# Kernel optimization log

Hardware: AMD Instinct MI355X
Metric: run time of the kernel (lower is better)

The kernel has to match this reference:

```python
import jax, jax.numpy as jnp
import numpy as np

B, C, H, W = 8, 3, 1024, 1024
N_SPOTS = int(H * W * 0.015)  # 15728, matches torch: n = int(H*W*0.015)
KSIZE, SIGMA = 5, 1.5
RMAX = 3  # max snow-box radius (torch.randint(1, 4))


def setup_inputs() -> dict:
    key = jax.random.key(0)
    k1, k2, k3, k4 = jax.random.split(key, 4)
    x = jax.random.uniform(k1, (B, C, H, W), dtype=jnp.float32)
    ys = jax.random.randint(k2, (B, N_SPOTS), 0, H)
    xs = jax.random.randint(k3, (B, N_SPOTS), 0, W)
    rs = jax.random.randint(k4, (B, N_SPOTS), 0, 3)  # radius = rs + 1 in {1,2,3}
    return {"x": x, "ys": ys, "xs": xs, "rs": rs}


def _snow_mask(ys, xs, rs, h, w):
    # Union of axis-aligned boxes: pixel (py,px) is snow iff some spot has
    # |py - y| <= r and |px - x| <= r (box clipping to the image is equivalent).
    b, n = ys.shape
    r = rs + 1  # radii 1..3
    d = jnp.arange(-RMAX, RMAX + 1)
    dy = jnp.repeat(d, 2 * RMAX + 1)  # [49]
    dx = jnp.tile(d, 2 * RMAX + 1)    # [49]
    yy = ys[:, :, None] + dy  # [B, n, 49]
    xx = xs[:, :, None] + dx
    valid = ((jnp.abs(dy) <= r[:, :, None]) & (jnp.abs(dx) <= r[:, :, None])
             & (yy >= 0) & (yy < h) & (xx >= 0) & (xx < w))
    yy = jnp.where(valid, yy, h)  # out-of-bounds sentinel -> dropped by scatter
    xx = jnp.where(valid, xx, w)
    b_idx = jnp.broadcast_to(jnp.arange(b)[:, None, None], yy.shape)
    mask = jnp.zeros((b, h, w), dtype=bool)
    mask = mask.at[b_idx, yy, xx].set(True, mode="drop")
    return mask


def _gauss_kernel():
    coords = jnp.arange(KSIZE, dtype=jnp.float32) - KSIZE // 2
    g = jnp.exp(-coords ** 2 / (2.0 * SIGMA ** 2))
    g = g / g.sum()
    return jnp.outer(g, g)  # [5, 5]


def reference(x, ys, xs, rs):
    b, c, h, w = x.shape
    mask = _snow_mask(ys, xs, rs, h, w)                   # [B, H, W]
    out = jnp.where(mask[:, None, :, :], jnp.float32(0.95), x)
    kernel = jnp.broadcast_to(_gauss_kernel(), (c, 1, KSIZE, KSIZE))  # depthwise OIHW
    pad = KSIZE // 2
    out = jax.lax.conv_general_dilated(
        out, kernel, window_strides=(1, 1), padding=[(pad, pad), (pad, pad)],
        dimension_numbers=("NCHW", "OIHW", "NCHW"), feature_group_count=c)
    return jnp.clip(out, 0.0, 1.0)
```

## Files before the change

kernel.cpp:

```cpp
#include <hip/hip_runtime.h>

#define BB 8
#define CC 3
#define HH 1024
#define WW 1024
#define NS 15728

#define G0 0.1200784f
#define G1 0.2338808f
#define G2 0.2920816f

__global__ __launch_bounds__(256) void snow_mask_kernel(
    const int* __restrict__ ys, const int* __restrict__ xs,
    const int* __restrict__ rs, unsigned int* __restrict__ mbits) {
  int s = blockIdx.x * 256 + threadIdx.x;
  if (s >= NS) return;
  int b = blockIdx.y;
  int idx = b * NS + s;
  int y = ys[idx];
  int x = xs[idx];
  int r = rs[idx] + 1;
  int x0 = max(x - r, 0), x1 = min(x + r, WW - 1);
  int y0 = max(y - r, 0), y1 = min(y + r, HH - 1);
  int w0 = x0 >> 5, w1 = x1 >> 5;
  unsigned int m0 = 0xFFFFFFFFu << (x0 & 31);
  unsigned int m1 = 0xFFFFFFFFu >> (31 - (x1 & 31));
  for (int py = y0; py <= y1; ++py) {
    unsigned int* rowp = mbits + ((unsigned)(b * HH + py) << 5);
    if (w0 == w1) {
      atomicOr(&rowp[w0], m0 & m1);
    } else {
      atomicOr(&rowp[w0], m0);
      atomicOr(&rowp[w1], m1);
    }
  }
}

__device__ __forceinline__ float hpass5(const float* row, int tx) {
  return G0 * (row[tx + 2] + row[tx + 6]) +
         G1 * (row[tx + 3] + row[tx + 5]) +
         G2 * row[tx + 4];
}

__global__ __launch_bounds__(256) void snow_blur_kernel(
    const float* __restrict__ x, const unsigned int* __restrict__ mbits,
    float* __restrict__ out) {
  __shared__ float tile[68][72];

  const int bz = blockIdx.z;
  const int b = bz / CC;
  const int bx = blockIdx.x, by = blockIdx.y;
  const int tid = threadIdx.x;
  const float* __restrict__ xp = x + (size_t)bz * (HH * WW);
  const unsigned int* __restrict__ mb = mbits + ((unsigned)(b * HH) << 5);

  const int gxbase = bx * 64 - 4;
  const int gybase = by * 64 - 2;

  const bool interior = (bx > 0) & (bx < 15) & (by > 0) & (by < 15);
  if (interior) {
#pragma unroll
    for (int k = 0; k < 5; ++k) {
      int i = tid + k * 256;
      if (i < 1224) {
        int r = i / 18;
        int c4 = i - r * 18;
        int gy = gybase + r;
        int gx = gxbase + c4 * 4;
        float4 v = *(const float4*)(xp + (size_t)gy * WW + gx);
        unsigned int mword = mb[(gy << 5) + (gx >> 5)];
        unsigned int bits = (mword >> (gx & 31)) & 0xFu;
        if (bits & 1u) v.x = 0.95f;
        if (bits & 2u) v.y = 0.95f;
        if (bits & 4u) v.z = 0.95f;
        if (bits & 8u) v.w = 0.95f;
        *(float4*)&tile[r][c4 * 4] = v;
      }
    }
  } else {
    for (int i = tid; i < 68 * 72; i += 256) {
      int r = i / 72;
      int c = i - r * 72;
      int gy = gybase + r;
      int gx = gxbase + c;
      float v = 0.f;
      if (gy >= 0 && gy < HH && gx >= 0 && gx < WW) {
        v = xp[(size_t)gy * WW + gx];
        if ((mb[(gy << 5) + (gx >> 5)] >> (gx & 31)) & 1u) v = 0.95f;
      }
      tile[r][c] = v;
    }
  }
  __syncthreads();

  const int tx = tid & 63;
  const int ty = tid >> 6;
  const int rbase = ty * 16;

  float h0 = hpass5(tile[rbase + 0], tx);
  float h1 = hpass5(tile[rbase + 1], tx);
  float h2 = hpass5(tile[rbase + 2], tx);
  float h3 = hpass5(tile[rbase + 3], tx);
  float h4 = hpass5(tile[rbase + 4], tx);

  size_t obase = (size_t)bz * (HH * WW) +
                 (size_t)(by * 64 + rbase) * WW +
                 (size_t)(bx * 64 + tx);
#pragma unroll
  for (int k = 0; k < 16; ++k) {
    float s = G0 * (h0 + h4) + G1 * (h1 + h3) + G2 * h2;
    s = fminf(fmaxf(s, 0.f), 1.f);
    out[obase + (size_t)k * WW] = s;
    h0 = h1; h1 = h2; h2 = h3; h3 = h4;
    if (k < 15) h4 = hpass5(tile[rbase + k + 5], tx);
  }
}

extern "C" void kernel_launch(void* const* d_in, const int* in_sizes, int n_in,
                              void* d_out, int out_size, void* d_ws, size_t ws_size,
                              hipStream_t stream) {
  const float* x = (const float*)d_in[0];
  const int* ys = (const int*)d_in[1];
  const int* xs = (const int*)d_in[2];
  const int* rs = (const int*)d_in[3];
  float* out = (float*)d_out;

  unsigned int* mbits = (unsigned int*)d_ws;
  hipMemsetAsync(mbits, 0, (size_t)BB * HH * WW / 8, stream);

  dim3 mgrid((NS + 255) / 256, BB);
  snow_mask_kernel<<<mgrid, 256, 0, stream>>>(ys, xs, rs, mbits);

  dim3 grid(WW / 64, HH / 64, BB * CC);
  snow_blur_kernel<<<grid, 256, 0, stream>>>(x, mbits, out);
}
```

Before: 230.9 us.

## Widen blur tiles to 128 columns with float4 per-thread outputs and clamped loads

The blur kernel now covers a 128x64 tile per block. Each thread computes four adjacent output columns over eight rows, using vectorized LDS reads and float4 global stores. The separate boundary path is replaced by clamped loads with a zero-out flag, and all ten loads are issued before the shared-memory writes so more memory requests are in flight. This cuts halo overhead and instruction count per output, but raises register pressure, which the added occupancy hint of 4 may constrain.

```diff
diff --git a/kernel.cpp b/kernel.cpp
--- a/kernel.cpp
+++ b/kernel.cpp
@@ -36,16 +36,13 @@
   }
 }
 
-__device__ __forceinline__ float hpass5(const float* row, int tx) {
-  return G0 * (row[tx + 2] + row[tx + 6]) +
-         G1 * (row[tx + 3] + row[tx + 5]) +
-         G2 * row[tx + 4];
-}
+#define TS 140
+#define NLOAD 2312
 
-__global__ __launch_bounds__(256) void snow_blur_kernel(
+__global__ __launch_bounds__(256, 4) void snow_blur_kernel(
     const float* __restrict__ x, const unsigned int* __restrict__ mbits,
     float* __restrict__ out) {
-  __shared__ float tile[68][72];
+  __shared__ float tile[68 * TS];
 
   const int bz = blockIdx.z;
   const int b = bz / CC;
@@ -54,65 +51,76 @@
   const float* __restrict__ xp = x + (size_t)bz * (HH * WW);
   const unsigned int* __restrict__ mb = mbits + ((unsigned)(b * HH) << 5);
 
-  const int gxbase = bx * 64 - 4;
+  const int gxbase = bx * 128 - 4;
   const int gybase = by * 64 - 2;
 
-  const bool interior = (bx > 0) & (bx < 15) & (by > 0) & (by < 15);
-  if (interior) {
+  float4 v[10];
+  unsigned int bits[10];
+  int lidx[10];
 #pragma unroll
-    for (int k = 0; k < 5; ++k) {
-      int i = tid + k * 256;
-      if (i < 1224) {
-        int r = i / 18;
-        int c4 = i - r * 18;
-        int gy = gybase + r;
-        int gx = gxbase + c4 * 4;
-        float4 v = *(const float4*)(xp + (size_t)gy * WW + gx);
-        unsigned int mword = mb[(gy << 5) + (gx >> 5)];
-        unsigned int bits = (mword >> (gx & 31)) & 0xFu;
-        if (bits & 1u) v.x = 0.95f;
-        if (bits & 2u) v.y = 0.95f;
-        if (bits & 4u) v.z = 0.95f;
-        if (bits & 8u) v.w = 0.95f;
-        *(float4*)&tile[r][c4 * 4] = v;
-      }
-    }
-  } else {
-    for (int i = tid; i < 68 * 72; i += 256) {
-      int r = i / 72;
-      int c = i - r * 72;
-      int gy = gybase + r;
-      int gx = gxbase + c;
-      float v = 0.f;
-      if (gy >= 0 && gy < HH && gx >= 0 && gx < WW) {
-        v = xp[(size_t)gy * WW + gx];
-        if ((mb[(gy << 5) + (gx >> 5)] >> (gx & 31)) & 1u) v = 0.95f;
-      }
-      tile[r][c] = v;
-    }
+  for (int k = 0; k < 10; ++k) {
+    int i = tid + k * 256;
+    i = i < (NLOAD - 1) ? i : (NLOAD - 1);
+    int r = i / 34;
+    int c4 = i - r * 34;
+    int gy = gybase + r;
+    int gx = gxbase + c4 * 4;
+    int gyc = min(max(gy, 0), HH - 1);
+    int gxc = min(max(gx, 0), WW - 4);
+    v[k] = *(const float4*)(xp + (size_t)gyc * WW + gxc);
+    unsigned int bm = (mb[(gyc << 5) + (gxc >> 5)] >> (gxc & 31)) & 0xFu;
+    if ((gy != gyc) | (gx != gxc)) bm = 16u;
+    bits[k] = bm;
+    lidx[k] = r * TS + c4 * 4;
+  }
+#pragma unroll
+  for (int k = 0; k < 10; ++k) {
+    float4 t = v[k];
+    unsigned int bm = bits[k];
+    if (bm & 1u) t.x = 0.95f;
+    if (bm & 2u) t.y = 0.95f;
+    if (bm & 4u) t.z = 0.95f;
+    if (bm & 8u) t.w = 0.95f;
+    if (bm & 16u) { t.x = 0.f; t.y = 0.f; t.z = 0.f; t.w = 0.f; }
+    *(float4*)&tile[lidx[k]] = t;
   }
   __syncthreads();
 
-  const int tx = tid & 63;
-  const int ty = tid >> 6;
-  const int rbase = ty * 16;
+  const int c = tid & 31;
+  const int ty = tid >> 5;
+  const float* trow = tile + (ty * 8) * TS + c * 4;
 
-  float h0 = hpass5(tile[rbase + 0], tx);
-  float h1 = hpass5(tile[rbase + 1], tx);
-  float h2 = hpass5(tile[rbase + 2], tx);
-  float h3 = hpass5(tile[rbase + 3], tx);
-  float h4 = hpass5(tile[rbase + 4], tx);
+  auto hrow = [&](int j, float4& h) {
+    const float* p = trow + j * TS;
+    float4 A = *(const float4*)(p);
+    float4 Bv = *(const float4*)(p + 4);
+    float2 Cv = *(const float2*)(p + 8);
+    h.x = G0 * (A.z + Bv.z) + G1 * (A.w + Bv.y) + G2 * Bv.x;
+    h.y = G0 * (A.w + Bv.w) + G1 * (Bv.x + Bv.z) + G2 * Bv.y;
+    h.z = G0 * (Bv.x + Cv.x) + G1 * (Bv.y + Bv.w) + G2 * Bv.z;
+    h.w = G0 * (Bv.y + Cv.y) + G1 * (Bv.z + Cv.x) + G2 * Bv.w;
+  };
 
-  size_t obase = (size_t)bz * (HH * WW) +
-                 (size_t)(by * 64 + rbase) * WW +
-                 (size_t)(bx * 64 + tx);
+  float4 h0, h1, h2, h3, h4;
+  hrow(0, h0); hrow(1, h1); hrow(2, h2); hrow(3, h3); hrow(4, h4);
+
+  float* op = out + (size_t)bz * (HH * WW) +
+              (size_t)(by * 64 + ty * 8) * WW + (bx * 128 + c * 4);
 #pragma unroll
-  for (int k = 0; k < 16; ++k) {
-    float s = G0 * (h0 + h4) + G1 * (h1 + h3) + G2 * h2;
-    s = fminf(fmaxf(s, 0.f), 1.f);
-    out[obase + (size_t)k * WW] = s;
+  for (int k = 0; k < 8; ++k) {
+    float4 s;
+    s.x = G0 * (h0.x + h4.x) + G1 * (h1.x + h3.x) + G2 * h2.x;
+    s.y = G0 * (h0.y + h4.y) + G1 * (h1.y + h3.y) + G2 * h2.y;
+    s.z = G0 * (h0.z + h4.z) + G1 * (h1.z + h3.z) + G2 * h2.z;
+    s.w = G0 * (h0.w + h4.w) + G1 * (h1.w + h3.w) + G2 * h2.w;
+    s.x = fminf(fmaxf(s.x, 0.f), 1.f);
+    s.y = fminf(fmaxf(s.y, 0.f), 1.f);
+    s.z = fminf(fmaxf(s.z, 0.f), 1.f);
+    s.w = fminf(fmaxf(s.w, 0.f), 1.f);
+    *(float4*)op = s;
+    op += WW;
     h0 = h1; h1 = h2; h2 = h3; h3 = h4;
-    if (k < 15) h4 = hpass5(tile[rbase + k + 5], tx);
+    if (k < 7) hrow(k + 5, h4);
   }
 }
 
@@ -131,6 +139,6 @@
   dim3 mgrid((NS + 255) / 256, BB);
   snow_mask_kernel<<<mgrid, 256, 0, stream>>>(ys, xs, rs, mbits);
 
-  dim3 grid(WW / 64, HH / 64, BB * CC);
+  dim3 grid(WW / 128, HH / 64, BB * CC);
   snow_blur_kernel<<<grid, 256, 0, stream>>>(x, mbits, out);
 }
```

New measurement: 210.2 us. -9.0%, faster.
